# Kernel optimization log

Hardware: AMD Instinct MI355X
Metric: run time of the kernel (lower is better)

The kernel has to match this reference:

```python
import jax, jax.numpy as jnp
import numpy as np

N, D, NUM_CLASSES = 8192, 1024, 128
ALPHA = 0.1
EPS = 1e-7


def setup_inputs() -> dict:
    key = jax.random.key(0)
    k1, k2 = jax.random.split(key)
    H = jax.random.normal(k1, (N, D), dtype=jnp.float32)
    labels = jax.random.randint(k2, (N,), 0, NUM_CLASSES, dtype=jnp.int64)
    return {"H": H, "labels": labels}


def reference(H, labels):
    n = H.shape[0]
    # squared-euclidean pairwise distances: ||x_i - x_j||^2
    x_norm = jnp.sum(H * H, axis=1)                      # [N]
    dists = x_norm[:, None] + x_norm[None, :] - 2.0 * (H @ H.T)
    dists = jnp.where(jnp.isnan(dists), 0.0, dists)      # dist[dist != dist] = 0
    dists = jnp.maximum(dists, 0.0)                      # clamp(0, inf)
    dists = jnp.maximum(dists, EPS)                      # clamp(min=1e-7)

    diffs = labels[None, :] - labels[:, None]            # [N, N]
    eye = jnp.eye(n, dtype=bool)
    mask_pos = (diffs == 0) & ~eye                       # same label, not self
    mask_neg = diffs != 0                                # different label

    # hardest positive: argmax over positive-masked distances
    anchor_positive_dist = jnp.where(mask_pos, dists, 0.0)
    hardest_positive_idx = jnp.argmax(anchor_positive_dist, axis=1)

    # hard negative: add row-max to non-negatives, take 2nd-smallest (k=1 partition)
    max_neg = jnp.max(dists, axis=1, keepdims=True)
    anchor_negative_dist = dists + max_neg * (1.0 - mask_neg.astype(dists.dtype))
    _, idx2 = jax.lax.top_k(-anchor_negative_dist, 2)    # two smallest per row
    hardest_negatives_idx = idx2[:, 1]

    rows = jnp.arange(n)
    hardest_positive_dist = dists[rows, hardest_positive_idx]
    hardest_negative_dist = dists[rows, hardest_negatives_idx]
    differences = hardest_positive_dist - hardest_negative_dist

    triplet_loss = jnp.maximum(differences + ALPHA, 0.0)  # final='plus', do_max=True
    relevant = triplet_loss > EPS                          # boolean mask (no grad)
    count = jnp.sum(relevant.astype(triplet_loss.dtype))
    return jnp.sum(jnp.where(relevant, triplet_loss, 0.0)) / count
```

## Files before the change

### kernel.cpp

```cpp
#include <hip/hip_runtime.h>
#include <hip/hip_bf16.h>
#include <stdint.h>

constexpr int Nn = 8192;
constexpr int Dd = 1024;
constexpr float kAlpha = 0.1f;
constexpr float kEps = 1e-7f;
constexpr float kInf = 3.0e38f;

constexpr int BM = 128, BN = 128, BK = 32;
constexpr int NB = Nn / BM;
constexpr int NPAIR = NB * (NB + 1) / 2;

using bfx8 = __attribute__((ext_vector_type(8))) __bf16;
using f32x4 = __attribute__((ext_vector_type(4))) float;

__device__ __forceinline__ unsigned short f2bf(float f) {
  union { float f; unsigned int u; } v; v.f = f;
  unsigned int u = v.u;
  u = u + 0x7fffu + ((u >> 16) & 1u);
  return (unsigned short)(u >> 16);
}

__device__ __forceinline__ void min2_insert(float& m1, float& m2, float x) {
  const float lo = fminf(m1, x);
  const float hi = fmaxf(m1, x);
  m1 = lo;
  m2 = fminf(m2, hi);
}

__device__ __forceinline__ void min2_merge(float& m1, float& m2, float o1, float o2) {
  m2 = fminf(fminf(m2, o2), fmaxf(m1, o1));
  m1 = fminf(m1, o1);
}

__global__ __launch_bounds__(256) void prep_kernel(const float* __restrict__ H,
                                                   unsigned short* __restrict__ Hb,
                                                   float* __restrict__ xn) {
  const int wave = threadIdx.x >> 6;
  const int lane = threadIdx.x & 63;
  const int row = blockIdx.x * 4 + wave;
  const float4* src = (const float4*)(H + (size_t)row * Dd);
  ushort4* dst = (ushort4*)(Hb + (size_t)row * Dd);
  float acc = 0.f;
#pragma unroll
  for (int i = 0; i < 4; ++i) {
    float4 v = src[lane + 64 * i];
    acc = fmaf(v.x, v.x, acc);
    acc = fmaf(v.y, v.y, acc);
    acc = fmaf(v.z, v.z, acc);
    acc = fmaf(v.w, v.w, acc);
    ushort4 o;
    o.x = f2bf(v.x); o.y = f2bf(v.y); o.z = f2bf(v.z); o.w = f2bf(v.w);
    dst[lane + 64 * i] = o;
  }
#pragma unroll
  for (int off = 32; off; off >>= 1) acc += __shfl_xor(acc, off, 64);
  if (lane == 0) xn[row] = acc;
}

__global__ __launch_bounds__(256, 2) void triplet_main(
    const unsigned short* __restrict__ Hb, const float* __restrict__ xn,
    const int* __restrict__ lab, float* __restrict__ wsMax,
    float* __restrict__ wsM1, float* __restrict__ wsM2) {
  __shared__ __align__(16) unsigned char smem[32768];

  const int tid = threadIdx.x;
  const int wave = tid >> 6;
  const int lane = tid & 63;
  const int quad = lane >> 4;
  const int l15 = lane & 15;
  const int wm = wave & 1;
  const int wn = wave >> 1;

  int b = blockIdx.x, I = 0;
  while (b >= NB - I) { b -= NB - I; ++I; }
  const int J = I + b;
  const bool diag = (I == J);

  const int rowBase = I * BM;
  const int colBase = J * BN;

  int lr[16]; float xr[16];
#pragma unroll
  for (int m = 0; m < 4; ++m)
#pragma unroll
    for (int r = 0; r < 4; ++r) {
      const int row = rowBase + wm * 64 + m * 16 + quad * 4 + r;
      lr[m * 4 + r] = lab[row];
      xr[m * 4 + r] = xn[row];
    }
  int lc[4]; float xc[4];
#pragma unroll
  for (int n = 0; n < 4; ++n) {
    const int col = colBase + wn * 64 + n * 16 + l15;
    lc[n] = lab[col];
    xc[n] = xn[col];
  }

  const int stRow = wave * 32 + (lane >> 2);
  const int stCol = (lane & 3) * 8;
  const unsigned short* gA = Hb + (size_t)(rowBase + stRow) * Dd + stCol;
  const unsigned short* gB = Hb + (size_t)(colBase + stRow) * Dd + stCol;

  auto stage = [&](int buf, int kt) {
    unsigned short* s = (unsigned short*)(smem + (buf << 14));
#pragma unroll
    for (int j = 0; j < 2; ++j) {
      __builtin_amdgcn_global_load_lds(
          (const __attribute__((address_space(1))) void*)(gA + j * 16 * Dd + kt),
          (__attribute__((address_space(3))) void*)&s[(wave * 2 + j) * 512],
          16, 0, 0);
      __builtin_amdgcn_global_load_lds(
          (const __attribute__((address_space(1))) void*)(gB + j * 16 * Dd + kt),
          (__attribute__((address_space(3))) void*)&s[4096 + (wave * 2 + j) * 512],
          16, 0, 0);
    }
  };

  f32x4 acc[4][4];
#pragma unroll
  for (int m = 0; m < 4; ++m)
#pragma unroll
    for (int n = 0; n < 4; ++n) acc[m][n] = {0.f, 0.f, 0.f, 0.f};

  auto compute = [&](int buf) {
    const unsigned short* s = (const unsigned short*)(smem + (buf << 14));
    bfx8 a[4], bb[4];
#pragma unroll
    for (int m = 0; m < 4; ++m)
      a[m] = *(const bfx8*)&s[(wm * 64 + m * 16 + l15) * BK + quad * 8];
#pragma unroll
    for (int n = 0; n < 4; ++n)
      bb[n] = *(const bfx8*)&s[4096 + (wn * 64 + n * 16 + l15) * BK + quad * 8];
#pragma unroll
    for (int m = 0; m < 4; ++m)
#pragma unroll
      for (int n = 0; n < 4; ++n)
        acc[m][n] = __builtin_amdgcn_mfma_f32_16x16x32_bf16(a[m], bb[n], acc[m][n], 0, 0, 0);
  };

  stage(0, 0);
  __syncthreads();

  constexpr int KIT = Dd / BK;
  for (int k0 = 0; k0 < KIT; k0 += 2) {
    stage(1, (k0 + 1) * BK);
    compute(0);
    __syncthreads();
    if (k0 + 2 < KIT) stage(0, (k0 + 2) * BK);
    compute(1);
    __syncthreads();
  }

  float maxp[16], mn1[16], mn2[16];
#pragma unroll
  for (int s = 0; s < 16; ++s) { maxp[s] = 0.f; mn1[s] = kInf; mn2[s] = kInf; }
  float tmaxp[4], tmn1[4], tmn2[4];
#pragma unroll
  for (int n = 0; n < 4; ++n) { tmaxp[n] = 0.f; tmn1[n] = kInf; tmn2[n] = kInf; }

  if (!diag) {
#pragma unroll
    for (int m = 0; m < 4; ++m)
#pragma unroll
      for (int n = 0; n < 4; ++n)
#pragma unroll
        for (int r = 0; r < 4; ++r) {
          const int s = m * 4 + r;
          const float d = fmaf(-2.f, acc[m][n][r], xr[s] + xc[n]);
          const bool eq = (lr[s] == lc[n]);
          const float pos = eq ? d : 0.f;
          const float dn = eq ? kInf : d;
          maxp[s] = fmaxf(maxp[s], pos);
          min2_insert(mn1[s], mn2[s], dn);
          tmaxp[n] = fmaxf(tmaxp[n], pos);
          min2_insert(tmn1[n], tmn2[n], dn);
        }
  } else {
#pragma unroll
    for (int m = 0; m < 4; ++m)
#pragma unroll
      for (int n = 0; n < 4; ++n)
#pragma unroll
        for (int r = 0; r < 4; ++r) {
          const int s = m * 4 + r;
          const bool selfp = (wm == wn) && (m == n) && (quad * 4 + r == l15);
          const float d = fmaf(-2.f, acc[m][n][r], xr[s] + xc[n]);
          const bool eq = (lr[s] == lc[n]);
          const float pos = (eq && !selfp) ? d : 0.f;
          const float dn = eq ? kInf : d;
          maxp[s] = fmaxf(maxp[s], pos);
          min2_insert(mn1[s], mn2[s], dn);
        }
  }

#pragma unroll
  for (int off = 1; off < 16; off <<= 1) {
#pragma unroll
    for (int s = 0; s < 16; ++s) {
      const float om = __shfl_xor(maxp[s], off, 64);
      const float o1 = __shfl_xor(mn1[s], off, 64);
      const float o2 = __shfl_xor(mn2[s], off, 64);
      maxp[s] = fmaxf(maxp[s], om);
      min2_merge(mn1[s], mn2[s], o1, o2);
    }
  }

  float* f = (float*)smem;
  float* rbm = f;
  float* rb1 = f + 128;
  float* rb2 = f + 256;
  float* tbm = f + 384;
  float* tb1 = tbm + 1024;
  float* tb2 = tb1 + 1024;

  if (wn == 1 && l15 == 0) {
#pragma unroll
    for (int m = 0; m < 4; ++m)
#pragma unroll
      for (int r = 0; r < 4; ++r) {
        const int s = m * 4 + r;
        const int local = wm * 64 + m * 16 + quad * 4 + r;
        rbm[local] = maxp[s];
        rb1[local] = mn1[s];
        rb2[local] = mn2[s];
      }
  }
#pragma unroll
  for (int n = 0; n < 4; ++n) {
    const int idx = (((wm * 2 + wn) * 4 + quad) * 4 + n) * 16 + l15;
    tbm[idx] = tmaxp[n];
    tb1[idx] = tmn1[n];
    tb2[idx] = tmn2[n];
  }
  __syncthreads();

  if (wn == 0 && l15 == 0) {
#pragma unroll
    for (int m = 0; m < 4; ++m)
#pragma unroll
      for (int r = 0; r < 4; ++r) {
        const int s = m * 4 + r;
        const int local = wm * 64 + m * 16 + quad * 4 + r;
        rbm[local] = fmaxf(maxp[s], rbm[local]);
        float a1 = mn1[s], a2 = mn2[s];
        min2_merge(a1, a2, rb1[local], rb2[local]);
        rb1[local] = a1;
        rb2[local] = a2;
      }
  }
  if (wm == 0 && !diag) {
    const int tn = lane >> 4;
    const int tl = lane & 15;
    float M = 0.f, a1 = kInf, a2 = kInf;
#pragma unroll
    for (int wm2 = 0; wm2 < 2; ++wm2)
#pragma unroll
      for (int q = 0; q < 4; ++q) {
        const int idx = (((wm2 * 2 + wn) * 4 + q) * 4 + tn) * 16 + tl;
        M = fmaxf(M, tbm[idx]);
        min2_merge(a1, a2, tb1[idx], tb2[idx]);
      }
    const size_t p = ((size_t)(J * NB + I)) * 128 + wn * 64 + lane;
    wsMax[p] = M;
    wsM1[p] = a1;
    wsM2[p] = a2;
  }
  __syncthreads();
  if (tid < 128) {
    const size_t p = ((size_t)(I * NB + J)) * 128 + tid;
    wsMax[p] = rbm[tid];
    wsM1[p] = rb1[tid];
    wsM2[p] = rb2[tid];
  }
}

__global__ __launch_bounds__(256) void merge_kernel(
    const float* __restrict__ wsMax, const float* __restrict__ wsM1,
    const float* __restrict__ wsM2, float* __restrict__ bsum,
    float* __restrict__ bcnt) {
  const int rl = threadIdx.x & 31;
  const int p = threadIdx.x >> 5;
  const int row = blockIdx.x * 32 + rl;
  const int bi = row >> 7;
  const int rr = row & 127;
  float mp = 0.f, m1 = kInf, m2 = kInf;
#pragma unroll
  for (int k = 0; k < 8; ++k) {
    const int bj = p * 8 + k;
    const size_t idx = ((size_t)(bi * NB + bj)) * 128 + rr;
    mp = fmaxf(mp, wsMax[idx]);
    min2_merge(m1, m2, wsM1[idx], wsM2[idx]);
  }
  __shared__ float sm[8][32], s1[8][32], s2[8][32];
  sm[p][rl] = mp; s1[p][rl] = m1; s2[p][rl] = m2;
  __syncthreads();
  float ls = 0.f, lc = 0.f;
  if (threadIdx.x < 32) {
    mp = sm[0][rl]; m1 = s1[0][rl]; m2 = s2[0][rl];
#pragma unroll
    for (int q = 1; q < 8; ++q) {
      mp = fmaxf(mp, sm[q][rl]);
      min2_merge(m1, m2, s1[q][rl], s2[q][rl]);
    }
    const float loss = fmaxf(mp - m2 + kAlpha, 0.f);
    ls = (loss > kEps) ? loss : 0.f;
    lc = (loss > kEps) ? 1.f : 0.f;
  }
  if (threadIdx.x < 64) {
#pragma unroll
    for (int off = 32; off; off >>= 1) {
      ls += __shfl_down(ls, off, 64);
      lc += __shfl_down(lc, off, 64);
    }
    if (threadIdx.x == 0) { bsum[blockIdx.x] = ls; bcnt[blockIdx.x] = lc; }
  }
}

__global__ __launch_bounds__(256) void final_kernel(const float* __restrict__ bsum,
                                                    const float* __restrict__ bcnt,
                                                    float* __restrict__ out) {
  float s = bsum[threadIdx.x];
  float c = bcnt[threadIdx.x];
#pragma unroll
  for (int off = 32; off; off >>= 1) {
    s += __shfl_down(s, off, 64);
    c += __shfl_down(c, off, 64);
  }
  __shared__ float ss[4], sc[4];
  const int w = threadIdx.x >> 6;
  if ((threadIdx.x & 63) == 0) { ss[w] = s; sc[w] = c; }
  __syncthreads();
  if (threadIdx.x == 0)
    out[0] = (ss[0] + ss[1] + ss[2] + ss[3]) / (sc[0] + sc[1] + sc[2] + sc[3]);
}

extern "C" void kernel_launch(void* const* d_in, const int* in_sizes, int n_in,
                              void* d_out, int out_size, void* d_ws, size_t ws_size,
                              hipStream_t stream) {
  (void)in_sizes; (void)n_in; (void)out_size; (void)ws_size;
  const float* H = (const float*)d_in[0];
  const int* lab = (const int*)d_in[1];
  float* out = (float*)d_out;

  char* ws = (char*)d_ws;
  unsigned short* Hb = (unsigned short*)ws;
  float* xn = (float*)(ws + (size_t)Nn * Dd * sizeof(unsigned short));
  float* wsMax = xn + Nn;
  float* wsM1 = wsMax + NB * NB * 128;
  float* wsM2 = wsM1 + NB * NB * 128;
  float* bsum = wsM2 + NB * NB * 128;
  float* bcnt = bsum + 256;

  prep_kernel<<<Nn / 4, 256, 0, stream>>>(H, Hb, xn);
  triplet_main<<<NPAIR, 256, 0, stream>>>(Hb, xn, lab, wsMax, wsM1, wsM2);
  merge_kernel<<<256, 256, 0, stream>>>(wsMax, wsM1, wsM2, bsum, bcnt);
  final_kernel<<<1, 256, 0, stream>>>(bsum, bcnt, out);
}
```

Before: 202.0 us.

## Replace direct global-to-LDS loads with register-staged four-deep prefetch pipeline

Drops the global_load_lds direct-to-LDS staging and instead loads tiles into registers four k-steps ahead, then writes them to double-buffered LDS one step before use. The aim is to hide global memory latency behind more MFMA work than the previous one-step-ahead double buffer allowed. In exchange it adds 16 uint4 registers per thread plus explicit LDS stores, which may reduce occupancy or add VALU/LDS store overhead. The loop also goes from two barriers per pair of k-steps to one barrier per k-step.

```diff
diff --git a/kernel.cpp b/kernel.cpp
--- a/kernel.cpp
+++ b/kernel.cpp
@@ -81,6 +81,67 @@
   const int rowBase = I * BM;
   const int colBase = J * BN;
 
+  const int c0 = tid, c1 = tid + 256;
+  const unsigned short* gA0 = Hb + (size_t)(rowBase + (c0 >> 2)) * Dd + (c0 & 3) * 8;
+  const unsigned short* gA1 = Hb + (size_t)(rowBase + (c1 >> 2)) * Dd + (c1 & 3) * 8;
+  const unsigned short* gB0 = Hb + (size_t)(colBase + (c0 >> 2)) * Dd + (c0 & 3) * 8;
+  const unsigned short* gB1 = Hb + (size_t)(colBase + (c1 >> 2)) * Dd + (c1 & 3) * 8;
+
+  constexpr int DEPTH = 4;
+  uint4 pa0[DEPTH], pa1[DEPTH], pb0[DEPTH], pb1[DEPTH];
+
+  auto ldg = [&](int set, int kt) {
+    pa0[set] = *(const uint4*)(gA0 + kt);
+    pa1[set] = *(const uint4*)(gA1 + kt);
+    pb0[set] = *(const uint4*)(gB0 + kt);
+    pb1[set] = *(const uint4*)(gB1 + kt);
+  };
+  auto sts = [&](int set, int buf) {
+    unsigned short* s = (unsigned short*)(smem + (buf << 14));
+    *(uint4*)(s + c0 * 8) = pa0[set];
+    *(uint4*)(s + c1 * 8) = pa1[set];
+    *(uint4*)(s + 4096 + c0 * 8) = pb0[set];
+    *(uint4*)(s + 4096 + c1 * 8) = pb1[set];
+  };
+
+  f32x4 acc[4][4];
+#pragma unroll
+  for (int m = 0; m < 4; ++m)
+#pragma unroll
+    for (int n = 0; n < 4; ++n) acc[m][n] = {0.f, 0.f, 0.f, 0.f};
+
+  auto compute = [&](int buf) {
+    const unsigned short* s = (const unsigned short*)(smem + (buf << 14));
+    bfx8 a[4], bb[4];
+#pragma unroll
+    for (int m = 0; m < 4; ++m)
+      a[m] = *(const bfx8*)&s[(wm * 64 + m * 16 + l15) * BK + quad * 8];
+#pragma unroll
+    for (int n = 0; n < 4; ++n)
+      bb[n] = *(const bfx8*)&s[4096 + (wn * 64 + n * 16 + l15) * BK + quad * 8];
+#pragma unroll
+    for (int m = 0; m < 4; ++m)
+#pragma unroll
+      for (int n = 0; n < 4; ++n)
+        acc[m][n] = __builtin_amdgcn_mfma_f32_16x16x32_bf16(a[m], bb[n], acc[m][n], 0, 0, 0);
+  };
+
+  ldg(0, 0 * BK);
+  ldg(1, 1 * BK);
+  ldg(2, 2 * BK);
+  ldg(3, 3 * BK);
+  sts(0, 0);
+  __syncthreads();
+
+  constexpr int KIT = Dd / BK;
+#pragma unroll 4
+  for (int k = 0; k < KIT; ++k) {
+    if (k + 1 < KIT) sts((k + 1) & 3, (k + 1) & 1);
+    if (k + 4 < KIT) ldg(k & 3, (k + 4) * BK);
+    compute(k & 1);
+    __syncthreads();
+  }
+
   int lr[16]; float xr[16];
 #pragma unroll
   for (int m = 0; m < 4; ++m)
@@ -96,61 +157,6 @@
     const int col = colBase + wn * 64 + n * 16 + l15;
     lc[n] = lab[col];
     xc[n] = xn[col];
-  }
-
-  const int stRow = wave * 32 + (lane >> 2);
-  const int stCol = (lane & 3) * 8;
-  const unsigned short* gA = Hb + (size_t)(rowBase + stRow) * Dd + stCol;
-  const unsigned short* gB = Hb + (size_t)(colBase + stRow) * Dd + stCol;
-
-  auto stage = [&](int buf, int kt) {
-    unsigned short* s = (unsigned short*)(smem + (buf << 14));
-#pragma unroll
-    for (int j = 0; j < 2; ++j) {
-      __builtin_amdgcn_global_load_lds(
-          (const __attribute__((address_space(1))) void*)(gA + j * 16 * Dd + kt),
-          (__attribute__((address_space(3))) void*)&s[(wave * 2 + j) * 512],
-          16, 0, 0);
-      __builtin_amdgcn_global_load_lds(
-          (const __attribute__((address_space(1))) void*)(gB + j * 16 * Dd + kt),
-          (__attribute__((address_space(3))) void*)&s[4096 + (wave * 2 + j) * 512],
-          16, 0, 0);
-    }
-  };
-
-  f32x4 acc[4][4];
-#pragma unroll
-  for (int m = 0; m < 4; ++m)
-#pragma unroll
-    for (int n = 0; n < 4; ++n) acc[m][n] = {0.f, 0.f, 0.f, 0.f};
-
-  auto compute = [&](int buf) {
-    const unsigned short* s = (const unsigned short*)(smem + (buf << 14));
-    bfx8 a[4], bb[4];
-#pragma unroll
-    for (int m = 0; m < 4; ++m)
-      a[m] = *(const bfx8*)&s[(wm * 64 + m * 16 + l15) * BK + quad * 8];
-#pragma unroll
-    for (int n = 0; n < 4; ++n)
-      bb[n] = *(const bfx8*)&s[4096 + (wn * 64 + n * 16 + l15) * BK + quad * 8];
-#pragma unroll
-    for (int m = 0; m < 4; ++m)
-#pragma unroll
-      for (int n = 0; n < 4; ++n)
-        acc[m][n] = __builtin_amdgcn_mfma_f32_16x16x32_bf16(a[m], bb[n], acc[m][n], 0, 0, 0);
-  };
-
-  stage(0, 0);
-  __syncthreads();
-
-  constexpr int KIT = Dd / BK;
-  for (int k0 = 0; k0 < KIT; k0 += 2) {
-    stage(1, (k0 + 1) * BK);
-    compute(0);
-    __syncthreads();
-    if (k0 + 2 < KIT) stage(0, (k0 + 2) * BK);
-    compute(1);
-    __syncthreads();
   }
 
   float maxp[16], mn1[16], mn2[16];
```

New measurement: 491.4 us. +143.2%, slower.

## Widen K tile, conflict-free LDS layout, XCD-aware block remap, single buffer

Applied to the files above, without the earlier changes.

The K tile grows from 32 to 64, so the loop runs half as many iterations. Staging now goes into separate A/B shared arrays with an 8-row interleaved layout meant to cut LDS bank conflicts on the MFMA operand reads. The block index is also permuted so consecutive pairs are spread across the 8 XCDs, which may improve L2 reuse. In exchange the double buffering is dropped: each iteration syncs, loads, syncs, then computes, so global-to-LDS copies no longer overlap with MFMA work.

```diff
diff --git a/kernel.cpp b/kernel.cpp
--- a/kernel.cpp
+++ b/kernel.cpp
@@ -8,9 +8,10 @@
 constexpr float kEps = 1e-7f;
 constexpr float kInf = 3.0e38f;
 
-constexpr int BM = 128, BN = 128, BK = 32;
+constexpr int BM = 128, BN = 128, BK = 64;
 constexpr int NB = Nn / BM;
 constexpr int NPAIR = NB * (NB + 1) / 2;
+constexpr int KIT = Dd / BK;
 
 using bfx8 = __attribute__((ext_vector_type(8))) __bf16;
 using f32x4 = __attribute__((ext_vector_type(4))) float;
@@ -63,7 +64,8 @@
     const unsigned short* __restrict__ Hb, const float* __restrict__ xn,
     const int* __restrict__ lab, float* __restrict__ wsMax,
     float* __restrict__ wsM1, float* __restrict__ wsM2) {
-  __shared__ __align__(16) unsigned char smem[32768];
+  __shared__ __align__(16) unsigned short As[BM * BK];
+  __shared__ __align__(16) unsigned short Bs[BN * BK];
 
   const int tid = threadIdx.x;
   const int wave = tid >> 6;
@@ -73,13 +75,75 @@
   const int wm = wave & 1;
   const int wn = wave >> 1;
 
-  int b = blockIdx.x, I = 0;
+  const int pid = (blockIdx.x & 7) * (NPAIR / 8) + (blockIdx.x >> 3);
+  int b = pid, I = 0;
   while (b >= NB - I) { b -= NB - I; ++I; }
   const int J = I + b;
   const bool diag = (I == J);
 
   const int rowBase = I * BM;
   const int colBase = J * BN;
+
+  const int rlo = lane & 7;
+  const int q8 = (lane >> 3) * 8;
+
+  auto stageAB = [&](int kt) {
+#pragma unroll
+    for (int j = 0; j < 4; ++j) {
+      const int i = wave * 4 + j;
+      const unsigned short* ga =
+          Hb + (size_t)(rowBase + i * 8 + rlo) * Dd + kt + q8;
+      __builtin_amdgcn_global_load_lds(
+          (const __attribute__((address_space(1))) void*)ga,
+          (__attribute__((address_space(3))) void*)&As[i * 512 + lane * 8],
+          16, 0, 0);
+      const unsigned short* gb =
+          Hb + (size_t)(colBase + i * 8 + rlo) * Dd + kt + q8;
+      __builtin_amdgcn_global_load_lds(
+          (const __attribute__((address_space(1))) void*)gb,
+          (__attribute__((address_space(3))) void*)&Bs[i * 512 + lane * 8],
+          16, 0, 0);
+    }
+  };
+
+  const int aHi = wm * 8 + (l15 >> 3);
+  const int bHi = wn * 8 + (l15 >> 3);
+  const int rl7 = l15 & 7;
+
+  f32x4 acc[4][4];
+#pragma unroll
+  for (int m = 0; m < 4; ++m)
+#pragma unroll
+    for (int n = 0; n < 4; ++n) acc[m][n] = {0.f, 0.f, 0.f, 0.f};
+
+  auto compute = [&]() {
+#pragma unroll
+    for (int h = 0; h < 2; ++h) {
+      bfx8 a[4], bb[4];
+#pragma unroll
+      for (int m = 0; m < 4; ++m)
+        a[m] = *(const bfx8*)&As[((aHi + m * 2) * 64 + (h * 4 + quad) * 8 + rl7) * 8];
+#pragma unroll
+      for (int n = 0; n < 4; ++n)
+        bb[n] = *(const bfx8*)&Bs[((bHi + n * 2) * 64 + (h * 4 + quad) * 8 + rl7) * 8];
+#pragma unroll
+      for (int m = 0; m < 4; ++m)
+#pragma unroll
+        for (int n = 0; n < 4; ++n)
+          acc[m][n] = __builtin_amdgcn_mfma_f32_16x16x32_bf16(a[m], bb[n], acc[m][n], 0, 0, 0);
+    }
+  };
+
+  stageAB(0);
+  __syncthreads();
+  compute();
+#pragma unroll 1
+  for (int it = 1; it < KIT; ++it) {
+    __syncthreads();
+    stageAB(it * BK);
+    __syncthreads();
+    compute();
+  }
 
   int lr[16]; float xr[16];
 #pragma unroll
@@ -96,61 +160,6 @@
     const int col = colBase + wn * 64 + n * 16 + l15;
     lc[n] = lab[col];
     xc[n] = xn[col];
-  }
-
-  const int stRow = wave * 32 + (lane >> 2);
-  const int stCol = (lane & 3) * 8;
-  const unsigned short* gA = Hb + (size_t)(rowBase + stRow) * Dd + stCol;
-  const unsigned short* gB = Hb + (size_t)(colBase + stRow) * Dd + stCol;
-
-  auto stage = [&](int buf, int kt) {
-    unsigned short* s = (unsigned short*)(smem + (buf << 14));
-#pragma unroll
-    for (int j = 0; j < 2; ++j) {
-      __builtin_amdgcn_global_load_lds(
-          (const __attribute__((address_space(1))) void*)(gA + j * 16 * Dd + kt),
-          (__attribute__((address_space(3))) void*)&s[(wave * 2 + j) * 512],
-          16, 0, 0);
-      __builtin_amdgcn_global_load_lds(
-          (const __attribute__((address_space(1))) void*)(gB + j * 16 * Dd + kt),
-          (__attribute__((address_space(3))) void*)&s[4096 + (wave * 2 + j) * 512],
-          16, 0, 0);
-    }
-  };
-
-  f32x4 acc[4][4];
-#pragma unroll
-  for (int m = 0; m < 4; ++m)
-#pragma unroll
-    for (int n = 0; n < 4; ++n) acc[m][n] = {0.f, 0.f, 0.f, 0.f};
-
-  auto compute = [&](int buf) {
-    const unsigned short* s = (const unsigned short*)(smem + (buf << 14));
-    bfx8 a[4], bb[4];
-#pragma unroll
-    for (int m = 0; m < 4; ++m)
-      a[m] = *(const bfx8*)&s[(wm * 64 + m * 16 + l15) * BK + quad * 8];
-#pragma unroll
-    for (int n = 0; n < 4; ++n)
-      bb[n] = *(const bfx8*)&s[4096 + (wn * 64 + n * 16 + l15) * BK + quad * 8];
-#pragma unroll
-    for (int m = 0; m < 4; ++m)
-#pragma unroll
-      for (int n = 0; n < 4; ++n)
-        acc[m][n] = __builtin_amdgcn_mfma_f32_16x16x32_bf16(a[m], bb[n], acc[m][n], 0, 0, 0);
-  };
-
-  stage(0, 0);
-  __syncthreads();
-
-  constexpr int KIT = Dd / BK;
-  for (int k0 = 0; k0 < KIT; k0 += 2) {
-    stage(1, (k0 + 1) * BK);
-    compute(0);
-    __syncthreads();
-    if (k0 + 2 < KIT) stage(0, (k0 + 2) * BK);
-    compute(1);
-    __syncthreads();
   }
 
   float maxp[16], mn1[16], mn2[16];
@@ -207,7 +216,8 @@
     }
   }
 
-  float* f = (float*)smem;
+  __syncthreads();
+  float* f = (float*)As;
   float* rbm = f;
   float* rb1 = f + 128;
   float* rb2 = f + 256;
```

Result: slower. 247.2 us (+22.4%).
